# Performance work log

Measured on AMD Instinct MI355X. Metric: run time of the kernel, lower is better.

Reference implementation:

```python
import jax, jax.numpy as jnp
import numpy as np

HEAD = 8
AGENT = 64  # agent_q_num = agent_kv_num = 8**2
DIM = 512


def _heads(t, head=HEAD):
    b, n, c = t.shape
    return t.reshape(b, n, head, c // head).transpose(0, 2, 1, 3)  # (b,h,n,d)


def _attn(q, k, v, pe, scale):
    # post-softmax additive bias (the non-standard part that breaks SDPA fusion)
    s = jax.nn.softmax(jnp.einsum('bhnd,bhmd->bhnm', q, k) * scale, axis=-1) + pe
    o = jnp.einsum('bhnm,bhmd->bhnd', s, v)
    b, h, n, d = o.shape
    return o.transpose(0, 2, 1, 3).reshape(b, n, h * d)


def _mlp(x, w1, b1, w2, b2):
    return jax.nn.silu(x @ w1 + b1) @ w2 + b2


def setup_inputs() -> dict:
    key = jax.random.key(0)
    ks = jax.random.split(key, 32)
    d = DIM
    inp = {
        'x': jax.random.normal(ks[0], (8, 64, 64, d), jnp.float32),
        'learnable_q': jax.random.normal(ks[1], (1, AGENT, d), jnp.float32) * 0.02,
        'learnable_kv': jax.random.normal(ks[2], (1, AGENT, d), jnp.float32) * 0.02,
        'pe1': jax.random.normal(ks[3], (1, HEAD, 1, AGENT), jnp.float32) * 0.02,
        'pe2': jax.random.normal(ks[4], (1, HEAD, AGENT, 1), jnp.float32) * 0.02,
        'w_q': jax.random.normal(ks[5], (d, d), jnp.float32) * (d ** -0.5),
        'b_q': jax.random.normal(ks[6], (d,), jnp.float32) * 0.02,
        'w_kvx': jax.random.normal(ks[7], (d, 2 * d), jnp.float32) * (d ** -0.5),
        'b_kvx': jax.random.normal(ks[8], (2 * d,), jnp.float32) * 0.02,
        'w_kvy': jax.random.normal(ks[9], (d, 2 * d), jnp.float32) * (d ** -0.5),
        'b_kvy': jax.random.normal(ks[10], (2 * d,), jnp.float32) * 0.02,
        'w_q2': jax.random.normal(ks[11], (d, d), jnp.float32) * (d ** -0.5),
        'b_q2': jax.random.normal(ks[12], (d,), jnp.float32) * 0.02,
        'f1w1': jax.random.normal(ks[13], (d, d), jnp.float32) * (d ** -0.5),
        'f1b1': jax.random.normal(ks[14], (d,), jnp.float32) * 0.02,
        'f1w2': jax.random.normal(ks[15], (d, d), jnp.float32) * (d ** -0.5),
        'f1b2': jax.random.normal(ks[16], (d,), jnp.float32) * 0.02,
        'f2w1': jax.random.normal(ks[17], (d, d), jnp.float32) * (d ** -0.5),
        'f2b1': jax.random.normal(ks[18], (d,), jnp.float32) * 0.02,
        'f2w2': jax.random.normal(ks[19], (d, d), jnp.float32) * (d ** -0.5),
        'f2b2': jax.random.normal(ks[20], (d,), jnp.float32) * 0.02,
    }
    return inp


def reference(x, learnable_q, learnable_kv, pe1, pe2, w_q, b_q, w_kvx, b_kvx,
              w_kvy, b_kvy, w_q2, b_q2, f1w1, f1b1, f1w2, f1b2,
              f2w1, f2b1, f2w2, f2b2):
    b, h, w, c = x.shape
    d = c // HEAD
    scale = d ** -0.5
    xf = x.reshape(b, h * w, c)

    # stage 1: image tokens attend to learnable proxy kv tokens
    q = _heads(xf @ w_q2 + b_q2)                                   # (b,H,hw,d)
    kv = jnp.broadcast_to(learnable_kv, (b, AGENT, c)) @ w_kvy + b_kvy
    k, v = jnp.split(kv, 2, axis=-1)
    out = _attn(q, _heads(k), _heads(v), pe1, scale)               # (b,hw,c)
    out = _mlp(out, f1w1, f1b1, f1w2, f1b2) + xf
    mskip = out

    # stage 2: learnable proxy queries attend to image tokens
    q2 = _heads(jnp.broadcast_to(learnable_q, (b, AGENT, c)) @ w_q + b_q)
    kv = out @ w_kvx + b_kvx
    k, v = jnp.split(kv, 2, axis=-1)
    fin = _attn(q2, _heads(k), _heads(v), pe2, scale)              # (b,AGENT,c)
    fin = _mlp(fin, f2w1, f2b1, f2w2, f2b2)

    # nearest-neighbor upsample 8x8 agent grid back to (h,w)
    s = int(AGENT ** 0.5)
    fin = fin.reshape(b, s, s, c)
    fin = jnp.repeat(jnp.repeat(fin, h // s, axis=1), w // s, axis=2)
    return fin + mskip.reshape(b, h, w, c) + x
```

## Files before the change

kernel.cpp:

```cpp
#include <hip/hip_runtime.h>
#include <stdint.h>

typedef unsigned short ub16;
typedef __attribute__((ext_vector_type(8))) short short8;
typedef __attribute__((ext_vector_type(4))) float f32x4;
typedef __attribute__((ext_vector_type(4))) unsigned short us4v;

__device__ __forceinline__ float bf2f(ub16 u) {
  union { unsigned int i; float f; } v; v.i = ((unsigned int)u) << 16; return v.f;
}
__device__ __forceinline__ ub16 f2bf(float f) {
  union { float f; unsigned int i; } v; v.f = f;
  return (ub16)((v.i + 0x7FFFu + ((v.i >> 16) & 1u)) >> 16);
}
__device__ __forceinline__ f32x4 zero4() { f32x4 v = {0.f, 0.f, 0.f, 0.f}; return v; }
__device__ __forceinline__ f32x4 mfma16(short8 a, short8 b, f32x4 c) {
  return __builtin_amdgcn_mfma_f32_16x16x32_bf16(a, b, c, 0, 0, 0);
}
__device__ __forceinline__ float rmax16(float x) {
  x = fmaxf(x, __shfl_xor(x, 1)); x = fmaxf(x, __shfl_xor(x, 2));
  x = fmaxf(x, __shfl_xor(x, 4)); x = fmaxf(x, __shfl_xor(x, 8)); return x;
}
__device__ __forceinline__ float rsum16(float x) {
  x += __shfl_xor(x, 1); x += __shfl_xor(x, 2);
  x += __shfl_xor(x, 4); x += __shfl_xor(x, 8); return x;
}

__device__ __forceinline__ void gload16(const ub16* g, ub16* l) {
  __builtin_amdgcn_global_load_lds(
      (const __attribute__((address_space(1))) void*)g,
      (__attribute__((address_space(3))) void*)l, 16, 0, 0);
}

__device__ __forceinline__ void stage_tile(const ub16* __restrict__ src, ub16* ldsbase,
                                           int wid, int lane) {
  const int rr = lane >> 3;
  const int slog = (lane & 7) ^ rr;
#pragma unroll
  for (int c = 0; c < 4; ++c) {
    int chunk = wid * 4 + c;
    int row = chunk * 8 + rr;
    gload16(src + (size_t)row * 512 + slog * 8,
            (ub16*)((char*)ldsbase + chunk * 1024));
  }
}

__device__ __forceinline__ void gemm_compute(const ub16* Ab, const ub16* Bb, int wm, int wn,
                                             int l15, int lg, f32x4 acc[4][4]) {
#pragma unroll
  for (int kf = 0; kf < 2; ++kf) {
    short8 af[4], bfr[4];
#pragma unroll
    for (int mf = 0; mf < 4; ++mf) {
      int row = wm * 64 + mf * 16 + l15;
      af[mf] = *(const short8*)((const char*)Ab + row * 128 +
                                ((kf * 64 + lg * 16) ^ ((row & 7) << 4)));
    }
#pragma unroll
    for (int nf = 0; nf < 4; ++nf) {
      int row = wn * 64 + nf * 16 + l15;
      bfr[nf] = *(const short8*)((const char*)Bb + row * 128 +
                                 ((kf * 64 + lg * 16) ^ ((row & 7) << 4)));
    }
#pragma unroll
    for (int mf = 0; mf < 4; ++mf)
#pragma unroll
      for (int nf = 0; nf < 4; ++nf)
        acc[mf][nf] = mfma16(af[mf], bfr[nf], acc[mf][nf]);
  }
}

__device__ __forceinline__ void gemm_k512(const ub16* Ap, const ub16* Bp, ub16* lds,
                                          int wid, int lane, int wm, int wn, int l15, int lg,
                                          f32x4 acc[4][4]) {
  ub16* A0 = lds;          ub16* B0 = lds + 8192;
  ub16* A1 = lds + 16384;  ub16* B1 = lds + 24576;
  stage_tile(Ap, A0, wid, lane);
  stage_tile(Bp, B0, wid, lane);
#pragma unroll
  for (int kb = 0; kb < 8; kb += 2) {
    stage_tile(Ap + (kb + 1) * 64, A1, wid, lane);
    stage_tile(Bp + (kb + 1) * 64, B1, wid, lane);
    asm volatile("s_waitcnt vmcnt(8)" ::: "memory");
    __syncthreads();
    gemm_compute(A0, B0, wm, wn, l15, lg, acc);
    __syncthreads();
    if (kb + 2 < 8) {
      stage_tile(Ap + (kb + 2) * 64, A0, wid, lane);
      stage_tile(Bp + (kb + 2) * 64, B0, wid, lane);
      asm volatile("s_waitcnt vmcnt(8)" ::: "memory");
    } else {
      asm volatile("s_waitcnt vmcnt(0)" ::: "memory");
    }
    __syncthreads();
    gemm_compute(A1, B1, wm, wn, l15, lg, acc);
    __syncthreads();
  }
}

__device__ __forceinline__ void xcd_remap(int nx, int& m0, int& n0) {
  int bid = blockIdx.x, nwg = gridDim.x;
  int cpx = nwg >> 3;
  int wgid = (bid & 7) * cpx + (bid >> 3);
  n0 = (wgid % nx) * 128;
  m0 = (wgid / nx) * 128;
}

__global__ void k_cvt(const float* __restrict__ x, ub16* __restrict__ xb) {
  int i = blockIdx.x * 256 + threadIdx.x;
  f32x4 v = *(const f32x4*)&x[(size_t)i * 4];
  us4v o;
#pragma unroll
  for (int e = 0; e < 4; ++e) o[e] = f2bf(v[e]);
  *(us4v*)&xb[(size_t)i * 4] = o;
}

__global__ void k_prep_wt(const float* s0, const float* s1, const float* s2,
                          const float* s3, const float* s4,
                          ub16* d0, ub16* d1, ub16* d2, ub16* d3, ub16* d4) {
  const float* src; ub16* dst; int N;
  switch (blockIdx.z) {
    case 0: src = s0; dst = d0; N = 512; break;
    case 1: src = s1; dst = d1; N = 512; break;
    case 2: src = s2; dst = d2; N = 512; break;
    case 3: src = s3; dst = d3; N = 512; break;
    default: src = s4; dst = d4; N = 1024; break;
  }
  int n0 = blockIdx.x * 64, k0 = blockIdx.y * 64;
  if (n0 >= N) return;
  __shared__ float tile[64][65];
#pragma unroll
  for (int i = 0; i < 16; ++i) {
    int idx = i * 256 + threadIdx.x, r = idx >> 6, c = idx & 63;
    tile[r][c] = src[(size_t)(k0 + r) * N + n0 + c];
  }
  __syncthreads();
#pragma unroll
  for (int i = 0; i < 16; ++i) {
    int idx = i * 256 + threadIdx.x, r = idx >> 6, c = idx & 63;
    dst[(size_t)(n0 + r) * 512 + k0 + c] = f2bf(tile[c][r]);
  }
}

__global__ void k_prep_small(const float* __restrict__ lkv, const float* __restrict__ w_kvy,
                             const float* __restrict__ b_kvy, const float* __restrict__ lq,
                             const float* __restrict__ w_q, const float* __restrict__ b_q,
                             const float* __restrict__ pe1,
                             ub16* __restrict__ k1, ub16* __restrict__ v1T,
                             float* __restrict__ bias1, ub16* __restrict__ q2p) {
  int j = blockIdx.x, t = threadIdx.x;
  __shared__ float wcol[512];
  __shared__ float red[64];
  const float* W; const float* src; float bias; int NC, jj;
  if (j < 1024) { W = w_kvy; NC = 1024; src = lkv; jj = j;        bias = b_kvy[j]; }
  else          { W = w_q;   NC = 512;  src = lq;  jj = j - 1024; bias = b_q[jj]; }
#pragma unroll
  for (int e = 0; e < 8; ++e) wcol[t * 8 + e] = W[(size_t)(t * 8 + e) * NC + jj];
  __syncthreads();
  float acc = bias;
  for (int k = 0; k < 512; ++k) acc += src[(size_t)t * 512 + k] * wcol[k];
  if (j < 512) {
    int h = j >> 6, d = j & 63;
    k1[(size_t)(h * 64 + t) * 64 + d] = f2bf(acc * 0.125f);
  } else if (j < 1024) {
    int h = (j - 512) >> 6, d = (j - 512) & 63;
    v1T[(size_t)(h * 64 + d) * 64 + t] = f2bf(acc);
    red[t] = pe1[h * 64 + t] * acc;
    __syncthreads();
    for (int s = 32; s > 0; s >>= 1) { if (t < s) red[t] += red[t + s]; __syncthreads(); }
    if (t == 0) bias1[h * 64 + d] = red[0];
  } else {
    int h = jj >> 6, d = jj & 63;
    q2p[(size_t)(h * 64 + t) * 64 + d] = f2bf(acc * 0.125f);
  }
}

__global__ void k_prep_wqk(const float* __restrict__ w_q2, const float* __restrict__ b_q2,
                           const ub16* __restrict__ k1, ub16* __restrict__ WqkT,
                           float* __restrict__ biass) {
  int ha = blockIdx.x, h = ha >> 6, t = threadIdx.x;
  __shared__ float kr[64];
  kr[t] = bf2f(k1[(size_t)ha * 64 + t]);
  __syncthreads();
#pragma unroll
  for (int e = 0; e < 8; ++e) {
    int kin = t * 8 + e;
    float acc = 0.f;
    const float* wrow = &w_q2[(size_t)kin * 512 + h * 64];
    for (int d = 0; d < 64; ++d) acc += wrow[d] * kr[d];
    WqkT[(size_t)ha * 512 + kin] = f2bf(acc);
  }
  if (t == 0) {
    float acc = 0.f;
    for (int d = 0; d < 64; ++d) acc += b_q2[h * 64 + d] * kr[d];
    biass[ha] = acc;
  }
}

__global__ __launch_bounds__(256) void k_s1a(
    const ub16* __restrict__ xb, const ub16* __restrict__ WqkT,
    const float* __restrict__ biass, const ub16* __restrict__ v1T,
    const float* __restrict__ bias1, ub16* __restrict__ o1) {
  __shared__ ub16 lds[32768];
  const int tid = threadIdx.x, lane = tid & 63, wid = tid >> 6;
  const int wm = wid >> 1, wn = wid & 1;
  const int l15 = lane & 15, lg = lane >> 4;
  int m0, n0;
  xcd_remap(4, m0, n0);

  f32x4 acc[4][4];
#pragma unroll
  for (int a = 0; a < 4; ++a)
#pragma unroll
    for (int b = 0; b < 4; ++b) acc[a][b] = zero4();

  gemm_k512(xb + (size_t)m0 * 512, WqkT + (size_t)n0 * 512, lds,
            wid, lane, wm, wn, l15, lg, acc);

  __syncthreads();
  const int h = (n0 >> 6) + wn;
  char* Pl = (char*)lds + wid * 8192;
  float bsv[4];
#pragma unroll
  for (int nf = 0; nf < 4; ++nf) bsv[nf] = biass[h * 64 + nf * 16 + l15];
  float dinv[4][4];
#pragma unroll
  for (int mf = 0; mf < 4; ++mf) {
#pragma unroll
    for (int r = 0; r < 4; ++r) {
      float s0 = acc[mf][0][r] + bsv[0], s1 = acc[mf][1][r] + bsv[1];
      float s2 = acc[mf][2][r] + bsv[2], s3 = acc[mf][3][r] + bsv[3];
      float mx = rmax16(fmaxf(fmaxf(s0, s1), fmaxf(s2, s3)));
      float p0 = __expf(s0 - mx), p1 = __expf(s1 - mx);
      float p2 = __expf(s2 - mx), p3 = __expf(s3 - mx);
      float sm = rsum16(p0 + p1 + p2 + p3);
      dinv[mf][r] = 1.0f / sm;
      int tr = mf * 16 + lg * 4 + r;
      char* rb = Pl + tr * 128;
      int sw = (tr & 7) << 4;
      *(ub16*)(rb + (((0 * 16 + l15) * 2) ^ sw)) = f2bf(p0);
      *(ub16*)(rb + (((1 * 16 + l15) * 2) ^ sw)) = f2bf(p1);
      *(ub16*)(rb + (((2 * 16 + l15) * 2) ^ sw)) = f2bf(p2);
      *(ub16*)(rb + (((3 * 16 + l15) * 2) ^ sw)) = f2bf(p3);
    }
  }
  short8 pa[4][2], vb[4][2];
#pragma unroll
  for (int mf = 0; mf < 4; ++mf) {
    int row = mf * 16 + l15;
#pragma unroll
    for (int kf = 0; kf < 2; ++kf)
      pa[mf][kf] = *(const short8*)(Pl + row * 128 + ((kf * 64 + lg * 16) ^ ((row & 7) << 4)));
  }
#pragma unroll
  for (int nf = 0; nf < 4; ++nf)
#pragma unroll
    for (int kf = 0; kf < 2; ++kf)
      vb[nf][kf] = *(const short8*)&v1T[(size_t)(h * 64 + nf * 16 + l15) * 64 + kf * 32 + lg * 8];
  f32x4 oacc[4][4];
#pragma unroll
  for (int a = 0; a < 4; ++a)
#pragma unroll
    for (int b = 0; b < 4; ++b) oacc[a][b] = zero4();
#pragma unroll
  for (int kf = 0; kf < 2; ++kf)
#pragma unroll
    for (int mf = 0; mf < 4; ++mf)
#pragma unroll
      for (int nf = 0; nf < 4; ++nf)
        oacc[mf][nf] = mfma16(pa[mf][kf], vb[nf][kf], oacc[mf][nf]);
  float b1v[4];
#pragma unroll
  for (int nf = 0; nf < 4; ++nf) b1v[nf] = bias1[h * 64 + nf * 16 + l15];
#pragma unroll
  for (int mf = 0; mf < 4; ++mf)
#pragma unroll
    for (int nf = 0; nf < 4; ++nf)
#pragma unroll
      for (int r = 0; r < 4; ++r) {
        float val = oacc[mf][nf][r] * dinv[mf][r] + b1v[nf];
        o1[(size_t)(m0 + wm * 64 + mf * 16 + lg * 4 + r) * 512 + h * 64 + nf * 16 + l15] = f2bf(val);
      }
}

__global__ __launch_bounds__(256) void k_mlp1a(
    const ub16* __restrict__ o1, const ub16* __restrict__ W1T,
    const float* __restrict__ b1, ub16* __restrict__ h1) {
  __shared__ ub16 lds[32768];
  const int tid = threadIdx.x, lane = tid & 63, wid = tid >> 6;
  const int wm = wid >> 1, wn = wid & 1;
  const int l15 = lane & 15, lg = lane >> 4;
  int m0, n0;
  xcd_remap(4, m0, n0);
  f32x4 acc[4][4];
#pragma unroll
  for (int a = 0; a < 4; ++a)
#pragma unroll
    for (int b = 0; b < 4; ++b) acc[a][b] = zero4();
  gemm_k512(o1 + (size_t)m0 * 512, W1T + (size_t)n0 * 512, lds,
            wid, lane, wm, wn, l15, lg, acc);
#pragma unroll
  for (int nf = 0; nf < 4; ++nf) {
    int n = n0 + wn * 64 + nf * 16 + l15;
    float bb = b1[n];
#pragma unroll
    for (int mf = 0; mf < 4; ++mf)
#pragma unroll
      for (int r = 0; r < 4; ++r) {
        float v = acc[mf][nf][r] + bb;
        v = v / (1.0f + __expf(-v));
        int m = m0 + wm * 64 + mf * 16 + lg * 4 + r;
        h1[(size_t)m * 512 + n] = f2bf(v);
      }
  }
}

__global__ __launch_bounds__(256) void k_mlp1b(
    const ub16* __restrict__ h1, const ub16* __restrict__ W2T,
    const float* __restrict__ b2, ub16* __restrict__ xb_mskip) {
  __shared__ ub16 lds[32768];
  const int tid = threadIdx.x, lane = tid & 63, wid = tid >> 6;
  const int wm = wid >> 1, wn = wid & 1;
  const int l15 = lane & 15, lg = lane >> 4;
  int m0, n0;
  xcd_remap(4, m0, n0);
  f32x4 acc[4][4];
#pragma unroll
  for (int a = 0; a < 4; ++a)
#pragma unroll
    for (int b = 0; b < 4; ++b) acc[a][b] = zero4();
  gemm_k512(h1 + (size_t)m0 * 512, W2T + (size_t)n0 * 512, lds,
            wid, lane, wm, wn, l15, lg, acc);
#pragma unroll
  for (int nf = 0; nf < 4; ++nf) {
    int n = n0 + wn * 64 + nf * 16 + l15;
    float bb = b2[n];
#pragma unroll
    for (int mf = 0; mf < 4; ++mf)
#pragma unroll
      for (int r = 0; r < 4; ++r) {
        int m = m0 + wm * 64 + mf * 16 + lg * 4 + r;
        size_t idx = (size_t)m * 512 + n;
        float val = acc[mf][nf][r] + bb + bf2f(xb_mskip[idx]);
        xb_mskip[idx] = f2bf(val);
      }
  }
}

__global__ __launch_bounds__(256) void k_mlp2b(
    const ub16* __restrict__ h2, const ub16* __restrict__ W2T,
    const float* __restrict__ b2, float* __restrict__ fin) {
  __shared__ ub16 lds[32768];
  const int tid = threadIdx.x, lane = tid & 63, wid = tid >> 6;
  const int wm = wid >> 1, wn = wid & 1;
  const int l15 = lane & 15, lg = lane >> 4;
  int m0, n0;
  xcd_remap(4, m0, n0);
  f32x4 acc[4][4];
#pragma unroll
  for (int a = 0; a < 4; ++a)
#pragma unroll
    for (int b = 0; b < 4; ++b) acc[a][b] = zero4();
  gemm_k512(h2 + (size_t)m0 * 512, W2T + (size_t)n0 * 512, lds,
            wid, lane, wm, wn, l15, lg, acc);
#pragma unroll
  for (int nf = 0; nf < 4; ++nf) {
    int n = n0 + wn * 64 + nf * 16 + l15;
    float bb = b2[n];
#pragma unroll
    for (int mf = 0; mf < 4; ++mf)
#pragma unroll
      for (int r = 0; r < 4; ++r) {
        int m = m0 + wm * 64 + mf * 16 + lg * 4 + r;
        fin[(size_t)m * 512 + n] = acc[mf][nf][r] + bb;
      }
  }
}

__global__ __launch_bounds__(256) void k_g4(
    const ub16* __restrict__ mskip_bf, const ub16* __restrict__ WT,
    const float* __restrict__ bias, ub16* __restrict__ Kb, ub16* __restrict__ VTb) {
  __shared__ ub16 lds[32768];
  const int tid = threadIdx.x, lane = tid & 63, wid = tid >> 6;
  const int wm = wid >> 1, wn = wid & 1;
  const int l15 = lane & 15, lg = lane >> 4;
  int m0, n0;
  xcd_remap(8, m0, n0);
  f32x4 acc[4][4];
#pragma unroll
  for (int a = 0; a < 4; ++a)
#pragma unroll
    for (int b = 0; b < 4; ++b) acc[a][b] = zero4();
  gemm_k512(mskip_bf + (size_t)m0 * 512, WT + (size_t)n0 * 512, lds,
            wid, lane, wm, wn, l15, lg, acc);
  const int ncb = n0 + wn * 64;
  if (n0 < 512) {
    const int hh = ncb >> 6;
#pragma unroll
    for (int mf = 0; mf < 4; ++mf)
#pragma unroll
      for (int r = 0; r < 4; ++r) {
        int m = m0 + wm * 64 + mf * 16 + lg * 4 + r;
        int b = m >> 12, t = m & 4095;
#pragma unroll
        for (int nf = 0; nf < 4; ++nf) {
          int d = nf * 16 + l15;
          Kb[((size_t)(b * 8 + hh) * 4096 + t) * 64 + d] = f2bf(acc[mf][nf][r] + bias[ncb + d]);
        }
      }
  } else {
    const int hv = (ncb >> 6) - 8;
#pragma unroll
    for (int mf = 0; mf < 4; ++mf) {
      int m4 = m0 + wm * 64 + mf * 16 + lg * 4;
      int b = m4 >> 12, t = m4 & 4095;
#pragma unroll
      for (int nf = 0; nf < 4; ++nf) {
        int d = nf * 16 + l15;
        float bb = bias[ncb + d];
        us4v pk;
#pragma unroll
        for (int r = 0; r < 4; ++r) pk[r] = f2bf(acc[mf][nf][r] + bb);
        *(us4v*)&VTb[((size_t)(b * 8 + hv) * 64 + d) * 4096 + t] = pk;
      }
    }
  }
}

__global__ __launch_bounds__(256) void k_attn2(
    const ub16* __restrict__ q2p, const ub16* __restrict__ Kb, const ub16* __restrict__ VTb,
    float* __restrict__ m_part, float* __restrict__ l_part,
    float* __restrict__ cs_part, float* __restrict__ o_part) {
  const int tid = threadIdx.x, lane = tid & 63, wid = tid >> 6;
  const int l15 = lane & 15, lg = lane >> 4;
  const int b = blockIdx.z, h = blockIdx.y;
  const int split = blockIdx.x * 4 + wid;
  __shared__ ub16 plds[4 * 64 * 40];
  ub16* pl = plds + wid * 64 * 40;
  short8 qa[4][2];
#pragma unroll
  for (int mf = 0; mf < 4; ++mf)
#pragma unroll
    for (int kf = 0; kf < 2; ++kf)
      qa[mf][kf] = *(const short8*)&q2p[(size_t)(h * 64 + mf * 16 + l15) * 64 + kf * 32 + lg * 8];
  float mr[4][4], lr[4][4], cs[4] = {0.f, 0.f, 0.f, 0.f};
  f32x4 oa[4][4];
#pragma unroll
  for (int a = 0; a < 4; ++a)
#pragma unroll
    for (int r = 0; r < 4; ++r) { mr[a][r] = -1e30f; lr[a][r] = 0.f; }
#pragma unroll
  for (int a = 0; a < 4; ++a)
#pragma unroll
    for (int n = 0; n < 4; ++n) oa[a][n] = zero4();
  const size_t kbase = (size_t)(b * 8 + h) * 4096 * 64;
  const size_t vbase = (size_t)(b * 8 + h) * 64 * 4096;
  for (int c = 0; c < 8; ++c) {
    int tb = split * 256 + c * 32;
    short8 kbf[2][2];
#pragma unroll
    for (int nf = 0; nf < 2; ++nf)
#pragma unroll
      for (int kf = 0; kf < 2; ++kf)
        kbf[nf][kf] = *(const short8*)&Kb[kbase + (size_t)(tb + nf * 16 + l15) * 64 + kf * 32 + lg * 8];
    f32x4 sc[4][2];
#pragma unroll
    for (int a = 0; a < 4; ++a)
#pragma unroll
      for (int n = 0; n < 2; ++n) sc[a][n] = zero4();
#pragma unroll
    for (int kf = 0; kf < 2; ++kf)
#pragma unroll
      for (int mf = 0; mf < 4; ++mf)
#pragma unroll
        for (int nf = 0; nf < 2; ++nf)
          sc[mf][nf] = mfma16(qa[mf][kf], kbf[nf][kf], sc[mf][nf]);
    float al[4][4];
#pragma unroll
    for (int mf = 0; mf < 4; ++mf)
#pragma unroll
      for (int r = 0; r < 4; ++r) {
        float cm = rmax16(fmaxf(sc[mf][0][r], sc[mf][1][r]));
        float nm = fmaxf(mr[mf][r], cm);
        float a_ = __expf(mr[mf][r] - nm);
        float p0 = __expf(sc[mf][0][r] - nm), p1 = __expf(sc[mf][1][r] - nm);
        float rs = rsum16(p0 + p1);
        lr[mf][r] = lr[mf][r] * a_ + rs;
        mr[mf][r] = nm;
        al[mf][r] = a_;
        int ar = mf * 16 + lg * 4 + r;
        char* rb = (char*)pl + ar * 80;
        *(ub16*)(rb + (0 * 16 + l15) * 2) = f2bf(p0);
        *(ub16*)(rb + (1 * 16 + l15) * 2) = f2bf(p1);
      }
#pragma unroll
    for (int mf = 0; mf < 4; ++mf)
#pragma unroll
      for (int nf = 0; nf < 4; ++nf)
#pragma unroll
        for (int r = 0; r < 4; ++r) oa[mf][nf][r] *= al[mf][r];
    short8 pa[4], vb[4];
#pragma unroll
    for (int mf = 0; mf < 4; ++mf)
      pa[mf] = *(const short8*)((char*)pl + (mf * 16 + l15) * 80 + lg * 16);
#pragma unroll
    for (int nf = 0; nf < 4; ++nf) {
      vb[nf] = *(const short8*)&VTb[vbase + (size_t)(nf * 16 + l15) * 4096 + tb + lg * 8];
#pragma unroll
      for (int e = 0; e < 8; ++e) cs[nf] += bf2f((ub16)vb[nf][e]);
    }
#pragma unroll
    for (int mf = 0; mf < 4; ++mf)
#pragma unroll
      for (int nf = 0; nf < 4; ++nf)
        oa[mf][nf] = mfma16(pa[mf], vb[nf], oa[mf][nf]);
  }
#pragma unroll
  for (int nf = 0; nf < 4; ++nf) {
    cs[nf] += __shfl_xor(cs[nf], 16);
    cs[nf] += __shfl_xor(cs[nf], 32);
  }
  const int pidx = (b * 8 + h) * 16 + split;
  if (lg == 0) {
#pragma unroll
    for (int nf = 0; nf < 4; ++nf) cs_part[(size_t)pidx * 64 + nf * 16 + l15] = cs[nf];
  }
  if (l15 == 0) {
#pragma unroll
    for (int mf = 0; mf < 4; ++mf)
#pragma unroll
      for (int r = 0; r < 4; ++r) {
        int a = mf * 16 + lg * 4 + r;
        m_part[(size_t)pidx * 64 + a] = mr[mf][r];
        l_part[(size_t)pidx * 64 + a] = lr[mf][r];
      }
  }
#pragma unroll
  for (int mf = 0; mf < 4; ++mf)
#pragma unroll
    for (int nf = 0; nf < 4; ++nf)
#pragma unroll
      for (int r = 0; r < 4; ++r) {
        int a = mf * 16 + lg * 4 + r, d = nf * 16 + l15;
        o_part[(size_t)pidx * 4096 + a * 64 + d] = oa[mf][nf][r];
      }
}

__global__ __launch_bounds__(256) void k_combine(
    const float* __restrict__ m_part, const float* __restrict__ l_part,
    const float* __restrict__ cs_part, const float* __restrict__ o_part,
    const float* __restrict__ pe2, ub16* __restrict__ fin0) {
  int bh = blockIdx.x, b = bh >> 3, h = bh & 7;
  int t = threadIdx.x;
  __shared__ float wsp[16][64];
  __shared__ float linv[64];
  __shared__ float cst[64];
  int base = bh * 16;
  if (t < 64) {
    int a = t;
    float M = -1e30f;
    for (int s = 0; s < 16; ++s) M = fmaxf(M, m_part[(size_t)(base + s) * 64 + a]);
    float L = 0.f;
    for (int s = 0; s < 16; ++s) {
      float w = __expf(m_part[(size_t)(base + s) * 64 + a] - M);
      wsp[s][a] = w;
      L += l_part[(size_t)(base + s) * 64 + a] * w;
    }
    linv[a] = 1.0f / L;
  } else if (t < 128) {
    int d = t - 64;
    float c = 0.f;
    for (int s = 0; s < 16; ++s) c += cs_part[(size_t)(base + s) * 64 + d];
    cst[d] = c;
  }
  __syncthreads();
#pragma unroll
  for (int e0 = 0; e0 < 4096; e0 += 256) {
    int e = e0 + t, a = e >> 6, d = e & 63;
    float acc = 0.f;
#pragma unroll
    for (int s = 0; s < 16; ++s) acc += o_part[(size_t)(base + s) * 4096 + e] * wsp[s][a];
    float val = acc * linv[a] + pe2[h * 64 + a] * cst[d];
    fin0[(size_t)(b * 64 + a) * 512 + h * 64 + d] = f2bf(val);
  }
}

__global__ void k_final(const float* __restrict__ x, const float* __restrict__ fin,
                        const ub16* __restrict__ mskip_bf, float* __restrict__ out) {
  int i = blockIdx.x * 256 + threadIdx.x;
  int e = i * 4;
  int c = e & 511, j = (e >> 9) & 63, ii = (e >> 15) & 63, b = e >> 21;
  f32x4 xv = *(const f32x4*)&x[(size_t)e];
  us4v mv = *(const us4v*)&mskip_bf[(size_t)e];
  f32x4 fv = *(const f32x4*)&fin[(size_t)((b * 64 + (ii >> 3) * 8 + (j >> 3)) << 9) + c];
  f32x4 r;
#pragma unroll
  for (int q = 0; q < 4; ++q) r[q] = xv[q] + fv[q] + bf2f(mv[q]);
  *(f32x4*)&out[(size_t)e] = r;
}

extern "C" void kernel_launch(void* const* d_in, const int* in_sizes, int n_in,
                              void* d_out, int out_size, void* d_ws, size_t ws_size,
                              hipStream_t stream) {
  const float* x     = (const float*)d_in[0];
  const float* lq    = (const float*)d_in[1];
  const float* lkv   = (const float*)d_in[2];
  const float* pe1   = (const float*)d_in[3];
  const float* pe2   = (const float*)d_in[4];
  const float* w_q   = (const float*)d_in[5];
  const float* b_q   = (const float*)d_in[6];
  const float* w_kvx = (const float*)d_in[7];
  const float* b_kvx = (const float*)d_in[8];
  const float* w_kvy = (const float*)d_in[9];
  const float* b_kvy = (const float*)d_in[10];
  const float* w_q2  = (const float*)d_in[11];
  const float* b_q2  = (const float*)d_in[12];
  const float* f1w1  = (const float*)d_in[13];
  const float* f1b1  = (const float*)d_in[14];
  const float* f1w2  = (const float*)d_in[15];
  const float* f1b2  = (const float*)d_in[16];
  const float* f2w1  = (const float*)d_in[17];
  const float* f2b1  = (const float*)d_in[18];
  const float* f2w2  = (const float*)d_in[19];
  const float* f2b2  = (const float*)d_in[20];
  float* out = (float*)d_out;

  char* ws = (char*)d_ws;
  size_t off = 0;
  auto alloc = [&](size_t bytes) {
    char* p = ws + off;
    off += (bytes + 255) & ~(size_t)255;
    return p;
  };
  ub16* xb    = (ub16*)alloc((size_t)32768 * 512 * 2);
  ub16* o1    = (ub16*)alloc((size_t)32768 * 512 * 2);
  ub16* VTb   = (ub16*)alloc((size_t)64 * 64 * 4096 * 2);
  ub16* WqkT  = (ub16*)alloc((size_t)512 * 512 * 2);
  ub16* w1T   = (ub16*)alloc((size_t)512 * 512 * 2);
  ub16* w2T   = (ub16*)alloc((size_t)512 * 512 * 2);
  ub16* g1T   = (ub16*)alloc((size_t)512 * 512 * 2);
  ub16* g2T   = (ub16*)alloc((size_t)512 * 512 * 2);
  ub16* kvxT  = (ub16*)alloc((size_t)1024 * 512 * 2);
  ub16* k1    = (ub16*)alloc((size_t)8 * 64 * 64 * 2);
  ub16* v1T   = (ub16*)alloc((size_t)8 * 64 * 64 * 2);
  ub16* q2p   = (ub16*)alloc((size_t)8 * 64 * 64 * 2);
  float* bias1 = (float*)alloc(512 * 4);
  float* biass = (float*)alloc(512 * 4);
  float* m_part = (float*)alloc((size_t)1024 * 64 * 4);
  float* l_part = (float*)alloc((size_t)1024 * 64 * 4);
  float* cs_part = (float*)alloc((size_t)1024 * 64 * 4);
  float* o_part = (float*)alloc((size_t)1024 * 4096 * 4);
  ub16* fin0 = (ub16*)alloc((size_t)512 * 512 * 2);
  float* fin = (float*)alloc((size_t)512 * 512 * 4);
  ub16* h2 = (ub16*)alloc((size_t)512 * 512 * 2);
  ub16* Kbuf = o1;
  ub16* h1buf = VTb;
  ub16* mskip_bf = xb;
  (void)in_sizes; (void)n_in; (void)out_size; (void)ws_size;

  const int n4 = (8 * 64 * 64 * 512) / 4;

  k_cvt<<<n4 / 256, 256, 0, stream>>>(x, xb);
  k_prep_wt<<<dim3(16, 8, 5), 256, 0, stream>>>(f1w1, f1w2, f2w1, f2w2, w_kvx,
                                                w1T, w2T, g1T, g2T, kvxT);
  k_prep_small<<<1536, 64, 0, stream>>>(lkv, w_kvy, b_kvy, lq, w_q, b_q, pe1,
                                        k1, v1T, bias1, q2p);
  k_prep_wqk<<<512, 64, 0, stream>>>(w_q2, b_q2, k1, WqkT, biass);
  k_s1a<<<1024, 256, 0, stream>>>(xb, WqkT, biass, v1T, bias1, o1);
  k_mlp1a<<<1024, 256, 0, stream>>>(o1, w1T, f1b1, h1buf);
  k_mlp1b<<<1024, 256, 0, stream>>>(h1buf, w2T, f1b2, mskip_bf);
  k_g4<<<2048, 256, 0, stream>>>(mskip_bf, kvxT, b_kvx, Kbuf, VTb);
  k_attn2<<<dim3(4, 8, 8), 256, 0, stream>>>(q2p, Kbuf, VTb, m_part, l_part, cs_part, o_part);
  k_combine<<<64, 256, 0, stream>>>(m_part, l_part, cs_part, o_part, pe2, fin0);
  k_mlp1a<<<16, 256, 0, stream>>>(fin0, g1T, f2b1, h2);
  k_mlp2b<<<16, 256, 0, stream>>>(h2, g2T, f2b2, fin);
  k_final<<<n4 / 256, 256, 0, stream>>>(x, fin, mskip_bf, out);
}
```

Baseline: 378.0 us.

## Single-buffer the K=512 GEMM tiles to halve LDS, and widen the Wqk prep kernel

The shared GEMM main loop drops double buffering. It now stages one A/B tile per k-step, waits for all loads, then computes, so every GEMM kernel needs half the LDS. This could let more workgroups share a CU, but it gives up the overlap of global loads with MFMA compute, and the loop now stalls on every tile load. Separately, the Wqk prep kernel runs 256 threads per block with one or two outputs per thread and vectorized float4 weight loads, replacing 64 threads that each computed eight outputs.

```diff
diff --git a/kernel.cpp b/kernel.cpp
--- a/kernel.cpp
+++ b/kernel.cpp
@@ -73,27 +73,15 @@
 __device__ __forceinline__ void gemm_k512(const ub16* Ap, const ub16* Bp, ub16* lds,
                                           int wid, int lane, int wm, int wn, int l15, int lg,
                                           f32x4 acc[4][4]) {
-  ub16* A0 = lds;          ub16* B0 = lds + 8192;
-  ub16* A1 = lds + 16384;  ub16* B1 = lds + 24576;
-  stage_tile(Ap, A0, wid, lane);
-  stage_tile(Bp, B0, wid, lane);
-#pragma unroll
-  for (int kb = 0; kb < 8; kb += 2) {
-    stage_tile(Ap + (kb + 1) * 64, A1, wid, lane);
-    stage_tile(Bp + (kb + 1) * 64, B1, wid, lane);
-    asm volatile("s_waitcnt vmcnt(8)" ::: "memory");
+  ub16* A0 = lds;
+  ub16* B0 = lds + 8192;
+#pragma unroll
+  for (int kb = 0; kb < 8; ++kb) {
+    stage_tile(Ap + kb * 64, A0, wid, lane);
+    stage_tile(Bp + kb * 64, B0, wid, lane);
+    asm volatile("s_waitcnt vmcnt(0)" ::: "memory");
     __syncthreads();
     gemm_compute(A0, B0, wm, wn, l15, lg, acc);
-    __syncthreads();
-    if (kb + 2 < 8) {
-      stage_tile(Ap + (kb + 2) * 64, A0, wid, lane);
-      stage_tile(Bp + (kb + 2) * 64, B0, wid, lane);
-      asm volatile("s_waitcnt vmcnt(8)" ::: "memory");
-    } else {
-      asm volatile("s_waitcnt vmcnt(0)" ::: "memory");
-    }
-    __syncthreads();
-    gemm_compute(A1, B1, wm, wn, l15, lg, acc);
     __syncthreads();
   }
 }
@@ -175,19 +163,25 @@
   }
 }
 
-__global__ void k_prep_wqk(const float* __restrict__ w_q2, const float* __restrict__ b_q2,
-                           const ub16* __restrict__ k1, ub16* __restrict__ WqkT,
-                           float* __restrict__ biass) {
+__global__ __launch_bounds__(256) void k_prep_wqk(
+    const float* __restrict__ w_q2, const float* __restrict__ b_q2,
+    const ub16* __restrict__ k1, ub16* __restrict__ WqkT,
+    float* __restrict__ biass) {
   int ha = blockIdx.x, h = ha >> 6, t = threadIdx.x;
   __shared__ float kr[64];
-  kr[t] = bf2f(k1[(size_t)ha * 64 + t]);
+  if (t < 64) kr[t] = bf2f(k1[(size_t)ha * 64 + t]);
   __syncthreads();
 #pragma unroll
-  for (int e = 0; e < 8; ++e) {
-    int kin = t * 8 + e;
+  for (int i = 0; i < 2; ++i) {
+    int kin = t + i * 256;
+    const float* wrow = &w_q2[(size_t)kin * 512 + h * 64];
     float acc = 0.f;
-    const float* wrow = &w_q2[(size_t)kin * 512 + h * 64];
-    for (int d = 0; d < 64; ++d) acc += wrow[d] * kr[d];
+#pragma unroll
+    for (int d4 = 0; d4 < 16; ++d4) {
+      f32x4 wv = *(const f32x4*)&wrow[d4 * 4];
+      acc += wv[0] * kr[d4 * 4] + wv[1] * kr[d4 * 4 + 1] +
+             wv[2] * kr[d4 * 4 + 2] + wv[3] * kr[d4 * 4 + 3];
+    }
     WqkT[(size_t)ha * 512 + kin] = f2bf(acc);
   }
   if (t == 0) {
@@ -201,7 +195,7 @@
     const ub16* __restrict__ xb, const ub16* __restrict__ WqkT,
     const float* __restrict__ biass, const ub16* __restrict__ v1T,
     const float* __restrict__ bias1, ub16* __restrict__ o1) {
-  __shared__ ub16 lds[32768];
+  __shared__ ub16 lds[16384];
   const int tid = threadIdx.x, lane = tid & 63, wid = tid >> 6;
   const int wm = wid >> 1, wn = wid & 1;
   const int l15 = lane & 15, lg = lane >> 4;
@@ -286,7 +280,7 @@
 __global__ __launch_bounds__(256) void k_mlp1a(
     const ub16* __restrict__ o1, const ub16* __restrict__ W1T,
     const float* __restrict__ b1, ub16* __restrict__ h1) {
-  __shared__ ub16 lds[32768];
+  __shared__ ub16 lds[16384];
   const int tid = threadIdx.x, lane = tid & 63, wid = tid >> 6;
   const int wm = wid >> 1, wn = wid & 1;
   const int l15 = lane & 15, lg = lane >> 4;
@@ -318,7 +312,7 @@
 __global__ __launch_bounds__(256) void k_mlp1b(
     const ub16* __restrict__ h1, const ub16* __restrict__ W2T,
     const float* __restrict__ b2, ub16* __restrict__ xb_mskip) {
-  __shared__ ub16 lds[32768];
+  __shared__ ub16 lds[16384];
   const int tid = threadIdx.x, lane = tid & 63, wid = tid >> 6;
   const int wm = wid >> 1, wn = wid & 1;
   const int l15 = lane & 15, lg = lane >> 4;
@@ -350,7 +344,7 @@
 __global__ __launch_bounds__(256) void k_mlp2b(
     const ub16* __restrict__ h2, const ub16* __restrict__ W2T,
     const float* __restrict__ b2, float* __restrict__ fin) {
-  __shared__ ub16 lds[32768];
+  __shared__ ub16 lds[16384];
   const int tid = threadIdx.x, lane = tid & 63, wid = tid >> 6;
   const int wm = wid >> 1, wn = wid & 1;
   const int l15 = lane & 15, lg = lane >> 4;
@@ -380,7 +374,7 @@
 __global__ __launch_bounds__(256) void k_g4(
     const ub16* __restrict__ mskip_bf, const ub16* __restrict__ WT,
     const float* __restrict__ bias, ub16* __restrict__ Kb, ub16* __restrict__ VTb) {
-  __shared__ ub16 lds[32768];
+  __shared__ ub16 lds[16384];
   const int tid = threadIdx.x, lane = tid & 63, wid = tid >> 6;
   const int wm = wid >> 1, wn = wid & 1;
   const int l15 = lane & 15, lg = lane >> 4;
@@ -665,7 +659,7 @@
                                                 w1T, w2T, g1T, g2T, kvxT);
   k_prep_small<<<1536, 64, 0, stream>>>(lkv, w_kvy, b_kvy, lq, w_q, b_q, pe1,
                                         k1, v1T, bias1, q2p);
-  k_prep_wqk<<<512, 64, 0, stream>>>(w_q2, b_q2, k1, WqkT, biass);
+  k_prep_wqk<<<512, 256, 0, stream>>>(w_q2, b_q2, k1, WqkT, biass);
   k_s1a<<<1024, 256, 0, stream>>>(xb, WqkT, biass, v1T, bias1, o1);
   k_mlp1a<<<1024, 256, 0, stream>>>(o1, w1T, f1b1, h1buf);
   k_mlp1b<<<1024, 256, 0, stream>>>(h1buf, w2T, f1b2, mskip_bf);
```

Result: faster. 332.2 us (-12.1%).
